# Performance work log

Measured on AMD Instinct MI355X. Metric: run time of the kernel, lower is better.

Reference implementation:

```python
import jax, jax.numpy as jnp
import numpy as np

DIM = 768
HEADS = 12
DIM_HEAD = 64
INNER = HEADS * DIM_HEAD  # 768
SCALE = DIM_HEAD ** -0.5


def setup_inputs() -> dict:
    key = jax.random.key(0)
    k1, k2, k3, k4 = jax.random.split(key, 4)
    b, n = 8, 1024
    x = jax.random.normal(k1, (b, n, DIM), dtype=jnp.float32)
    # fused QKV projection, no bias: y = x @ w_qkv  -> [b, n, 3*inner]
    w_qkv = jax.random.normal(k2, (DIM, 3 * INNER), dtype=jnp.float32) * (DIM ** -0.5)
    # output projection with bias
    w_out = jax.random.normal(k3, (INNER, DIM), dtype=jnp.float32) * (INNER ** -0.5)
    b_out = jax.random.normal(k4, (DIM,), dtype=jnp.float32) * 0.02
    return {"x": x, "w_qkv": w_qkv, "w_out": w_out, "b_out": b_out}


def reference(x, w_qkv, w_out, b_out):
    b, n, _ = x.shape
    qkv = jnp.einsum('bnd,de->bne', x, w_qkv)  # [b, n, 3*inner]
    q, k, v = jnp.split(qkv, 3, axis=-1)
    # 'b n (h d) -> b h n d'
    def split_heads(t):
        return t.reshape(b, n, HEADS, DIM_HEAD).transpose(0, 2, 1, 3)
    q, k, v = split_heads(q), split_heads(k), split_heads(v)
    dots = jnp.einsum('bhid,bhjd->bhij', q, k) * SCALE  # [b, h, n, n]
    attn = jax.nn.softmax(dots, axis=-1)
    out = jnp.einsum('bhij,bhjd->bhid', attn, v)  # [b, h, n, d]
    out = out.transpose(0, 2, 1, 3).reshape(b, n, INNER)  # 'b h n d -> b n (h d)'
    return jnp.einsum('bne,ed->bnd', out, w_out) + b_out
```

## Files before the change

kernel.cpp:

```cpp
#include <hip/hip_runtime.h>

typedef unsigned short u16;
typedef __bf16 bf16x8 __attribute__((ext_vector_type(8)));
typedef float f32x4 __attribute__((ext_vector_type(4)));

__device__ inline u16 f2bf(float f) {
    union { float f; unsigned int u; } a; a.f = f;
    unsigned int u = a.u + 0x7fffu + ((a.u >> 16) & 1u);
    return (u16)(u >> 16);
}

__device__ __forceinline__ void cp16(const void* g, void* l) {
    __builtin_amdgcn_global_load_lds(
        (const __attribute__((address_space(1))) unsigned int*)g,
        (__attribute__((address_space(3))) unsigned int*)l, 16, 0, 0);
}

__global__ __launch_bounds__(256) void prep(
    const float* __restrict__ x, const float* __restrict__ wq,
    const float* __restrict__ wo, u16* __restrict__ xbf,
    u16* __restrict__ wtq, u16* __restrict__ wto)
{
    int bid = blockIdx.x;
    if (bid < 3072) {
        size_t base = ((size_t)bid * 256 + threadIdx.x) * 8;
        float4 f0 = *(const float4*)&x[base];
        float4 f1 = *(const float4*)&x[base + 4];
        union { u16 s[8]; uint4 v; } t;
        t.s[0]=f2bf(f0.x); t.s[1]=f2bf(f0.y); t.s[2]=f2bf(f0.z); t.s[3]=f2bf(f0.w);
        t.s[4]=f2bf(f1.x); t.s[5]=f2bf(f1.y); t.s[6]=f2bf(f1.z); t.s[7]=f2bf(f1.w);
        *(uint4*)&xbf[base] = t.v;
        return;
    }
    __shared__ u16 tile[32][33];
    const float* in; u16* outp; int N, bx, by;
    if (bid < 3072 + 1728) { int t = bid - 3072; in = wq; outp = wtq; N = 2304; bx = t % 72; by = t / 72; }
    else                   { int t = bid - 4800; in = wo; outp = wto; N = 768;  bx = t % 24; by = t / 24; }
    int n0 = bx * 32, k0 = by * 32;
    int tx = threadIdx.x & 31, ty = threadIdx.x >> 5;
    #pragma unroll
    for (int r = ty; r < 32; r += 8)
        tile[r][tx] = f2bf(in[(size_t)(k0 + r) * N + n0 + tx]);
    __syncthreads();
    #pragma unroll
    for (int r = ty; r < 32; r += 8)
        outp[(size_t)(n0 + r) * 768 + k0 + tx] = tile[tx][r];
}

__global__ __launch_bounds__(256) void gemm_qkv(
    const u16* __restrict__ A, const u16* __restrict__ Bt,
    u16* __restrict__ q_out, u16* __restrict__ k_out, u16* __restrict__ v_out)
{
    const int K = 768;
    __shared__ __align__(16) u16 As[2][128 * 64];
    __shared__ __align__(16) u16 Bs[2][128 * 64];

    int tid = threadIdx.x;
    int lane = tid & 63, wave = tid >> 6;
    int quad = lane >> 4, l16 = lane & 15;
    int wm = wave >> 1, wn = wave & 1;
    int id = blockIdx.x;
    int xcd = id & 7, j = id >> 3;
    int m0 = (((j & 7) << 3) + xcd) * 128;
    int n0 = (j >> 3) * 128;

    f32x4 acc[4][4];
    #pragma unroll
    for (int i = 0; i < 4; i++)
        #pragma unroll
        for (int jj = 0; jj < 4; jj++) acc[i][jj] = (f32x4){0.f, 0.f, 0.f, 0.f};

    int r0 = tid >> 3, cg = tid & 7;
    int g = cg ^ (r0 & 7);
    const u16* GA[4]; const u16* GB[4];
    #pragma unroll
    for (int it = 0; it < 4; it++) {
        GA[it] = A  + (size_t)(m0 + it * 32 + r0) * K + g * 8;
        GB[it] = Bt + (size_t)(n0 + it * 32 + r0) * K + g * 8;
    }

    #define STAGE_QKV(kt, b)                                          \
        _Pragma("unroll")                                             \
        for (int it = 0; it < 4; it++) {                              \
            cp16(GA[it] + (kt), &As[b][(it * 256 + tid) * 8]);        \
            cp16(GB[it] + (kt), &Bs[b][(it * 256 + tid) * 8]);        \
        }

    STAGE_QKV(0, 0)
    for (int i = 0; i < 12; i++) {
        int b = i & 1;
        if (i + 1 < 12) {
            STAGE_QKV((i + 1) * 64, b ^ 1)
            asm volatile("s_waitcnt vmcnt(8)" ::: "memory");
        } else {
            asm volatile("s_waitcnt vmcnt(0)" ::: "memory");
        }
        __builtin_amdgcn_s_barrier();
        bf16x8 af[2][4], bfr[2][4];
        #pragma unroll
        for (int ko = 0; ko < 2; ko++)
            #pragma unroll
            for (int x = 0; x < 4; x++) {
                int Ra = wm * 64 + x * 16 + l16;
                af[ko][x]  = *(const bf16x8*)&As[b][Ra * 64 + (((ko * 4 + quad) ^ (Ra & 7)) * 8)];
                int Rb = wn * 64 + x * 16 + l16;
                bfr[ko][x] = *(const bf16x8*)&Bs[b][Rb * 64 + (((ko * 4 + quad) ^ (Rb & 7)) * 8)];
            }
        #pragma unroll
        for (int ko = 0; ko < 2; ko++)
            #pragma unroll
            for (int x = 0; x < 4; x++)
                #pragma unroll
                for (int y = 0; y < 4; y++)
                    acc[x][y] = __builtin_amdgcn_mfma_f32_16x16x32_bf16(af[ko][x], bfr[ko][y], acc[x][y], 0, 0, 0);
        __builtin_amdgcn_s_barrier();
    }
    #undef STAGE_QKV

    int M0 = m0 + wm * 64, N0 = n0 + wn * 64;
    int part = N0 >= 1536 ? 2 : (N0 >= 768 ? 1 : 0);
    int h = (N0 - part * 768) >> 6;
    int b2 = M0 >> 10, npos0 = M0 & 1023;
    u16* ep = (wave < 2 ? As[0] : Bs[0]) + (wave & 1) * 4096;

    if (part != 2) {
        float scale = (part == 0) ? 0.18033688011112042f : 1.0f;
        u16* gbase = (part == 0 ? q_out : k_out) + (((size_t)(b2 * 12 + h) * 1024 + npos0) << 6);
        #pragma unroll
        for (int i = 0; i < 4; i++)
            #pragma unroll
            for (int jj = 0; jj < 4; jj++) {
                int dd = jj * 16 + l16;
                #pragma unroll
                for (int r = 0; r < 4; r++) {
                    int np = i * 16 + quad * 4 + r;
                    ep[np * 64 + (((dd >> 3) ^ (np & 7)) * 8) + (dd & 7)] =
                        f2bf(acc[i][jj][r] * scale);
                }
            }
        #pragma unroll
        for (int t = 0; t < 8; t++) {
            int idx = t * 512 + lane * 8;
            int np = idx >> 6;
            int slot = ((lane & 7) ^ (np & 7));
            uint4 v = *(const uint4*)&ep[np * 64 + slot * 8];
            *(uint4*)&gbase[idx] = v;
        }
    } else {
        #pragma unroll
        for (int i = 0; i < 4; i++)
            #pragma unroll
            for (int jj = 0; jj < 4; jj++) {
                int dd = jj * 16 + l16;
                int npg = i * 2 + (quad >> 1);
                int sub = (quad & 1) * 4;
                union { u16 s[4]; uint2 v; } pk;
                #pragma unroll
                for (int r = 0; r < 4; r++) pk.s[r] = f2bf(acc[i][jj][r]);
                *(uint2*)&ep[dd * 64 + ((npg ^ (dd & 7)) * 8) + sub] = pk.v;
            }
        #pragma unroll
        for (int t = 0; t < 8; t++) {
            int dd = t * 8 + (lane >> 3);
            int npg = lane & 7;
            uint4 v = *(const uint4*)&ep[dd * 64 + ((npg ^ (dd & 7)) * 8)];
            *(uint4*)&v_out[((size_t)((b2 * 12 + h) * 64 + dd)) * 1024 + npos0 + npg * 8] = v;
        }
    }
}

__global__ __launch_bounds__(256) void attn128(
    u16* __restrict__ QO, const u16* __restrict__ Kg, const u16* __restrict__ Vtg)
{
    __shared__ __align__(16) u16 Ks[2][64 * 64];
    __shared__ __align__(16) u16 Vs[2][64 * 64];

    int tid = threadIdx.x;
    int lane = tid & 63, wave = tid >> 6;
    int quad = lane >> 4, l16 = lane & 15;
    int id = blockIdx.x;
    int xcd = id & 7, j = id >> 3;
    int bh = xcd * 12 + (j >> 3);
    int q0 = (j & 7) * 128;
    const size_t head_base = (size_t)bh * 65536;

    size_t qoff[2];
    bf16x8 qf[2][2];
    #pragma unroll
    for (int qs = 0; qs < 2; qs++) {
        qoff[qs] = head_base + (size_t)(q0 + wave * 32 + qs * 16 + l16) * 64;
        qf[qs][0] = *(const bf16x8*)&QO[qoff[qs] + quad * 8];
        qf[qs][1] = *(const bf16x8*)&QO[qoff[qs] + 32 + quad * 8];
    }

    f32x4 Oacc[4][2];
    #pragma unroll
    for (int dt = 0; dt < 4; dt++)
        #pragma unroll
        for (int qs = 0; qs < 2; qs++) Oacc[dt][qs] = (f32x4){0.f, 0.f, 0.f, 0.f};
    f32x4 lacc[2];
    lacc[0] = (f32x4){0.f, 0.f, 0.f, 0.f};
    lacc[1] = (f32x4){0.f, 0.f, 0.f, 0.f};

    union { unsigned int w[4]; bf16x8 v; } ones;
    ones.w[0] = ones.w[1] = ones.w[2] = ones.w[3] = 0x3f803f80u;

    int srow = tid >> 3, sg = tid & 7;
    int gsK = sg ^ (srow & 7);
    const u16* GK[2];
    GK[0] = Kg + head_base + (size_t)(srow) * 64 + gsK * 8;
    GK[1] = Kg + head_base + (size_t)(32 + srow) * 64 + gsK * 8;
    const u16* GV[2];
    GV[0] = Vtg + head_base + (size_t)(srow) * 1024 + sg * 8;
    GV[1] = Vtg + head_base + (size_t)(32 + srow) * 1024 + sg * 8;
    int vwA[2], vwB[2];
    #pragma unroll
    for (int it = 0; it < 2; it++) {
        int r = it * 32 + srow;
        vwA[it] = r * 64 + (((2 * sg)     ^ (r & 15)) * 4);
        vwB[it] = r * 64 + (((2 * sg + 1) ^ (r & 15)) * 4);
    }

    uint4 v0a = *(const uint4*)GV[0];
    uint4 v0b = *(const uint4*)GV[1];
    cp16(GK[0], &Ks[0][(0 * 256 + tid) * 8]);
    cp16(GK[1], &Ks[0][(1 * 256 + tid) * 8]);
    { uint2 t;
      t.x = v0a.x; t.y = v0a.y; *(uint2*)&Vs[0][vwA[0]] = t;
      t.x = v0a.z; t.y = v0a.w; *(uint2*)&Vs[0][vwB[0]] = t;
      t.x = v0b.x; t.y = v0b.y; *(uint2*)&Vs[0][vwA[1]] = t;
      t.x = v0b.z; t.y = v0b.w; *(uint2*)&Vs[0][vwB[1]] = t; }
    asm volatile("s_waitcnt lgkmcnt(0)" ::: "memory");

    for (int i = 0; i < 16; i++) {
        int b = i & 1;
        uint4 vna, vnb;
        if (i + 1 < 16) {
            vna = *(const uint4*)(GV[0] + (i + 1) * 64);
            vnb = *(const uint4*)(GV[1] + (i + 1) * 64);
            cp16(GK[0] + (size_t)(i + 1) * 4096, &Ks[b ^ 1][(0 * 256 + tid) * 8]);
            cp16(GK[1] + (size_t)(i + 1) * 4096, &Ks[b ^ 1][(1 * 256 + tid) * 8]);
            asm volatile("s_waitcnt vmcnt(4)" ::: "memory");
        } else {
            asm volatile("s_waitcnt vmcnt(0)" ::: "memory");
        }
        __builtin_amdgcn_s_barrier();

        bf16x8 kf[4][2];
        #pragma unroll
        for (int nt = 0; nt < 4; nt++) {
            int R = nt * 16 + l16;
            kf[nt][0] = *(const bf16x8*)&Ks[b][R * 64 + ((quad       ^ (R & 7)) * 8)];
            kf[nt][1] = *(const bf16x8*)&Ks[b][R * 64 + (((quad + 4) ^ (R & 7)) * 8)];
        }
        f32x4 s4[4][2];
        #pragma unroll
        for (int nt = 0; nt < 4; nt++)
            #pragma unroll
            for (int qs = 0; qs < 2; qs++) {
                f32x4 s = (f32x4){0.f, 0.f, 0.f, 0.f};
                s = __builtin_amdgcn_mfma_f32_16x16x32_bf16(kf[nt][0], qf[qs][0], s, 0, 0, 0);
                s = __builtin_amdgcn_mfma_f32_16x16x32_bf16(kf[nt][1], qf[qs][1], s, 0, 0, 0);
                s4[nt][qs] = s;
            }

        float p[4][2][4];
        #pragma unroll
        for (int nt = 0; nt < 4; nt++)
            #pragma unroll
            for (int qs = 0; qs < 2; qs++)
                #pragma unroll
                for (int r = 0; r < 4; r++)
                    p[nt][qs][r] = __builtin_amdgcn_exp2f(s4[nt][qs][r]);

        if (i + 1 < 16) {
            asm volatile("s_waitcnt vmcnt(2)" ::: "memory");
            uint2 t;
            t.x = vna.x; t.y = vna.y; *(uint2*)&Vs[b ^ 1][vwA[0]] = t;
            t.x = vna.z; t.y = vna.w; *(uint2*)&Vs[b ^ 1][vwB[0]] = t;
            t.x = vnb.x; t.y = vnb.y; *(uint2*)&Vs[b ^ 1][vwA[1]] = t;
            t.x = vnb.z; t.y = vnb.w; *(uint2*)&Vs[b ^ 1][vwB[1]] = t;
        }

        __builtin_amdgcn_s_setprio(1);
        #pragma unroll
        for (int h = 0; h < 2; h++) {
            union { unsigned int w[4]; bf16x8 v; } pk[2];
            #pragma unroll
            for (int qs = 0; qs < 2; qs++) {
                asm("v_cvt_pk_bf16_f32 %0, %1, %2" : "=v"(pk[qs].w[0]) : "v"(p[2*h][qs][0]),     "v"(p[2*h][qs][1]));
                asm("v_cvt_pk_bf16_f32 %0, %1, %2" : "=v"(pk[qs].w[1]) : "v"(p[2*h][qs][2]),     "v"(p[2*h][qs][3]));
                asm("v_cvt_pk_bf16_f32 %0, %1, %2" : "=v"(pk[qs].w[2]) : "v"(p[2*h+1][qs][0]),   "v"(p[2*h+1][qs][1]));
                asm("v_cvt_pk_bf16_f32 %0, %1, %2" : "=v"(pk[qs].w[3]) : "v"(p[2*h+1][qs][2]),   "v"(p[2*h+1][qs][3]));
                lacc[qs] = __builtin_amdgcn_mfma_f32_16x16x32_bf16(ones.v, pk[qs].v, lacc[qs], 0, 0, 0);
            }
            int pbase = ((8 * h + quad) ^ l16) * 4;
            #pragma unroll
            for (int dt = 0; dt < 4; dt++) {
                int drow = dt * 16 + l16;
                union { u16 s[8]; bf16x8 v; } vk;
                *(uint2*)&vk.s[0] = *(const uint2*)&Vs[b][drow * 64 + pbase];
                *(uint2*)&vk.s[4] = *(const uint2*)&Vs[b][drow * 64 + (pbase ^ 16)];
                #pragma unroll
                for (int qs = 0; qs < 2; qs++)
                    Oacc[dt][qs] = __builtin_amdgcn_mfma_f32_16x16x32_bf16(vk.v, pk[qs].v, Oacc[dt][qs], 0, 0, 0);
            }
        }
        __builtin_amdgcn_s_setprio(0);

        asm volatile("s_waitcnt lgkmcnt(0)" ::: "memory");
        __builtin_amdgcn_s_barrier();
    }

    #pragma unroll
    for (int qs = 0; qs < 2; qs++) {
        float rl = __builtin_amdgcn_rcpf(lacc[qs][0]);
        #pragma unroll
        for (int dt = 0; dt < 4; dt++) {
            union { u16 s[4]; uint2 v; } ok;
            #pragma unroll
            for (int r = 0; r < 4; r++) ok.s[r] = f2bf(Oacc[dt][qs][r] * rl);
            *(uint2*)&QO[qoff[qs] + dt * 16 + quad * 4] = ok.v;
        }
    }
}

__global__ __launch_bounds__(256) void gemm_out(
    const u16* __restrict__ Qg, const u16* __restrict__ Bt,
    const float* __restrict__ bias, float* __restrict__ out)
{
    const int K = 768;
    __shared__ __align__(16) u16 As[2][128 * 64];
    __shared__ __align__(16) u16 Bs[2][128 * 64];

    int tid = threadIdx.x;
    int lane = tid & 63, wave = tid >> 6;
    int quad = lane >> 4, l16 = lane & 15;
    int wm = wave >> 1, wn = wave & 1;
    int id = blockIdx.x;
    int xcd = id & 7, j = id >> 3;
    int m0 = (((j & 7) << 3) + xcd) * 128;
    int n0 = (j >> 3) * 128;

    f32x4 acc[4][4];
    #pragma unroll
    for (int i = 0; i < 4; i++)
        #pragma unroll
        for (int jj = 0; jj < 4; jj++) acc[i][jj] = (f32x4){0.f, 0.f, 0.f, 0.f};

    int r0 = tid >> 3, cg = tid & 7;
    int g = cg ^ (r0 & 7);
    const u16* GA[4]; const u16* GB[4];
    #pragma unroll
    for (int it = 0; it < 4; it++) {
        int m = m0 + it * 32 + r0, b = m >> 10, npos = m & 1023;
        GA[it] = Qg + (((size_t)(b * 12) * 1024 + npos) << 6) + g * 8;
        GB[it] = Bt + (size_t)(n0 + it * 32 + r0) * K + g * 8;
    }

    #define STAGE_OUT(i2, b)                                              \
        _Pragma("unroll")                                                 \
        for (int it = 0; it < 4; it++) {                                  \
            cp16(GA[it] + (size_t)(i2) * 65536, &As[b][(it * 256 + tid) * 8]); \
            cp16(GB[it] + (i2) * 64,            &Bs[b][(it * 256 + tid) * 8]); \
        }

    STAGE_OUT(0, 0)
    for (int i = 0; i < 12; i++) {
        int b = i & 1;
        if (i + 1 < 12) {
            STAGE_OUT(i + 1, b ^ 1)
            asm volatile("s_waitcnt vmcnt(8)" ::: "memory");
        } else {
            asm volatile("s_waitcnt vmcnt(0)" ::: "memory");
        }
        __builtin_amdgcn_s_barrier();
        bf16x8 af[2][4], bfr[2][4];
        #pragma unroll
        for (int ko = 0; ko < 2; ko++)
            #pragma unroll
            for (int x = 0; x < 4; x++) {
                int Ra = wm * 64 + x * 16 + l16;
                af[ko][x]  = *(const bf16x8*)&As[b][Ra * 64 + (((ko * 4 + quad) ^ (Ra & 7)) * 8)];
                int Rb = wn * 64 + x * 16 + l16;
                bfr[ko][x] = *(const bf16x8*)&Bs[b][Rb * 64 + (((ko * 4 + quad) ^ (Rb & 7)) * 8)];
            }
        #pragma unroll
        for (int ko = 0; ko < 2; ko++)
            #pragma unroll
            for (int x = 0; x < 4; x++)
                #pragma unroll
                for (int y = 0; y < 4; y++)
                    acc[x][y] = __builtin_amdgcn_mfma_f32_16x16x32_bf16(af[ko][x], bfr[ko][y], acc[x][y], 0, 0, 0);
        __builtin_amdgcn_s_barrier();
    }
    #undef STAGE_OUT

    #pragma unroll
    for (int i = 0; i < 4; i++) {
        int mbase = m0 + wm * 64 + i * 16 + quad * 4;
        #pragma unroll
        for (int jj = 0; jj < 4; jj++) {
            int n = n0 + wn * 64 + jj * 16 + l16;
            float bv = bias[n];
            #pragma unroll
            for (int r = 0; r < 4; r++)
                out[(size_t)(mbase + r) * 768 + n] = acc[i][jj][r] + bv;
        }
    }
}

extern "C" void kernel_launch(void* const* d_in, const int* in_sizes, int n_in,
                              void* d_out, int out_size, void* d_ws, size_t ws_size,
                              hipStream_t stream) {
    const float* x     = (const float*)d_in[0];
    const float* w_qkv = (const float*)d_in[1];
    const float* w_out = (const float*)d_in[2];
    const float* b_out = (const float*)d_in[3];
    float* out = (float*)d_out;

    char* ws = (char*)d_ws;
    u16* wtq  = (u16*)(ws);
    u16* wto  = (u16*)(ws + 3538944);
    u16* Qbuf = (u16*)(ws + 4718592);
    u16* xbf  = (u16*)(ws + 17301504);
    u16* Kbuf = (u16*)d_out;
    u16* Vbuf = (u16*)d_out + 6291456;

    prep<<<dim3(5376), 256, 0, stream>>>(x, w_qkv, w_out, xbf, wtq, wto);
    gemm_qkv<<<dim3(1152), 256, 0, stream>>>(xbf, wtq, Qbuf, Kbuf, Vbuf);
    attn128<<<dim3(768), 256, 0, stream>>>(Qbuf, Kbuf, Vbuf);
    gemm_out<<<dim3(384), 256, 0, stream>>>(Qbuf, wto, b_out, out);
}
```

Before: 192.4 us.

## Prefetch V tiles two iterations ahead with register ping-pong in attention loop

Restructures the attention main loop into a manually unrolled pair of stages. V global loads are now issued two tiles ahead into alternating register sets, while K still goes one tile ahead via direct-to-LDS copies. The V LDS write for the next tile moves to the start of compute, so the in-loop vmcnt wait before the P·V stage goes away and global latency gets more cover. The cost is extra live registers for the second V buffer and more code size from the unrolling.

```diff
diff --git a/kernel.cpp b/kernel.cpp
--- a/kernel.cpp
+++ b/kernel.cpp
@@ -221,96 +221,115 @@
         vwB[it] = r * 64 + (((2 * sg + 1) ^ (r & 15)) * 4);
     }
 
-    uint4 v0a = *(const uint4*)GV[0];
-    uint4 v0b = *(const uint4*)GV[1];
+    uint4 vA0, vA1, vB0, vB1;
+
+    {
+        uint4 t0 = *(const uint4*)GV[0];
+        uint4 t1 = *(const uint4*)GV[1];
+        uint2 t;
+        t.x = t0.x; t.y = t0.y; *(uint2*)&Vs[0][vwA[0]] = t;
+        t.x = t0.z; t.y = t0.w; *(uint2*)&Vs[0][vwB[0]] = t;
+        t.x = t1.x; t.y = t1.y; *(uint2*)&Vs[0][vwA[1]] = t;
+        t.x = t1.z; t.y = t1.w; *(uint2*)&Vs[0][vwB[1]] = t;
+    }
+    vA0 = *(const uint4*)(GV[0] + 64);
+    vA1 = *(const uint4*)(GV[1] + 64);
     cp16(GK[0], &Ks[0][(0 * 256 + tid) * 8]);
     cp16(GK[1], &Ks[0][(1 * 256 + tid) * 8]);
-    { uint2 t;
-      t.x = v0a.x; t.y = v0a.y; *(uint2*)&Vs[0][vwA[0]] = t;
-      t.x = v0a.z; t.y = v0a.w; *(uint2*)&Vs[0][vwB[0]] = t;
-      t.x = v0b.x; t.y = v0b.y; *(uint2*)&Vs[0][vwA[1]] = t;
-      t.x = v0b.z; t.y = v0b.w; *(uint2*)&Vs[0][vwB[1]] = t; }
     asm volatile("s_waitcnt lgkmcnt(0)" ::: "memory");
 
-    for (int i = 0; i < 16; i++) {
-        int b = i & 1;
-        uint4 vna, vnb;
-        if (i + 1 < 16) {
-            vna = *(const uint4*)(GV[0] + (i + 1) * 64);
-            vnb = *(const uint4*)(GV[1] + (i + 1) * 64);
-            cp16(GK[0] + (size_t)(i + 1) * 4096, &Ks[b ^ 1][(0 * 256 + tid) * 8]);
-            cp16(GK[1] + (size_t)(i + 1) * 4096, &Ks[b ^ 1][(1 * 256 + tid) * 8]);
-            asm volatile("s_waitcnt vmcnt(4)" ::: "memory");
-        } else {
-            asm volatile("s_waitcnt vmcnt(0)" ::: "memory");
-        }
-        __builtin_amdgcn_s_barrier();
-
-        bf16x8 kf[4][2];
-        #pragma unroll
-        for (int nt = 0; nt < 4; nt++) {
-            int R = nt * 16 + l16;
-            kf[nt][0] = *(const bf16x8*)&Ks[b][R * 64 + ((quad       ^ (R & 7)) * 8)];
-            kf[nt][1] = *(const bf16x8*)&Ks[b][R * 64 + (((quad + 4) ^ (R & 7)) * 8)];
-        }
-        f32x4 s4[4][2];
-        #pragma unroll
-        for (int nt = 0; nt < 4; nt++)
-            #pragma unroll
-            for (int qs = 0; qs < 2; qs++) {
-                f32x4 s = (f32x4){0.f, 0.f, 0.f, 0.f};
-                s = __builtin_amdgcn_mfma_f32_16x16x32_bf16(kf[nt][0], qf[qs][0], s, 0, 0, 0);
-                s = __builtin_amdgcn_mfma_f32_16x16x32_bf16(kf[nt][1], qf[qs][1], s, 0, 0, 0);
-                s4[nt][qs] = s;
-            }
-
-        float p[4][2][4];
-        #pragma unroll
-        for (int nt = 0; nt < 4; nt++)
-            #pragma unroll
-            for (int qs = 0; qs < 2; qs++)
-                #pragma unroll
-                for (int r = 0; r < 4; r++)
-                    p[nt][qs][r] = __builtin_amdgcn_exp2f(s4[nt][qs][r]);
-
-        if (i + 1 < 16) {
-            asm volatile("s_waitcnt vmcnt(2)" ::: "memory");
-            uint2 t;
-            t.x = vna.x; t.y = vna.y; *(uint2*)&Vs[b ^ 1][vwA[0]] = t;
-            t.x = vna.z; t.y = vna.w; *(uint2*)&Vs[b ^ 1][vwB[0]] = t;
-            t.x = vnb.x; t.y = vnb.y; *(uint2*)&Vs[b ^ 1][vwA[1]] = t;
-            t.x = vnb.z; t.y = vnb.w; *(uint2*)&Vs[b ^ 1][vwB[1]] = t;
-        }
-
-        __builtin_amdgcn_s_setprio(1);
-        #pragma unroll
-        for (int h = 0; h < 2; h++) {
-            union { unsigned int w[4]; bf16x8 v; } pk[2];
-            #pragma unroll
-            for (int qs = 0; qs < 2; qs++) {
-                asm("v_cvt_pk_bf16_f32 %0, %1, %2" : "=v"(pk[qs].w[0]) : "v"(p[2*h][qs][0]),     "v"(p[2*h][qs][1]));
-                asm("v_cvt_pk_bf16_f32 %0, %1, %2" : "=v"(pk[qs].w[1]) : "v"(p[2*h][qs][2]),     "v"(p[2*h][qs][3]));
-                asm("v_cvt_pk_bf16_f32 %0, %1, %2" : "=v"(pk[qs].w[2]) : "v"(p[2*h+1][qs][0]),   "v"(p[2*h+1][qs][1]));
-                asm("v_cvt_pk_bf16_f32 %0, %1, %2" : "=v"(pk[qs].w[3]) : "v"(p[2*h+1][qs][2]),   "v"(p[2*h+1][qs][3]));
-                lacc[qs] = __builtin_amdgcn_mfma_f32_16x16x32_bf16(ones.v, pk[qs].v, lacc[qs], 0, 0, 0);
-            }
-            int pbase = ((8 * h + quad) ^ l16) * 4;
-            #pragma unroll
-            for (int dt = 0; dt < 4; dt++) {
-                int drow = dt * 16 + l16;
-                union { u16 s[8]; bf16x8 v; } vk;
-                *(uint2*)&vk.s[0] = *(const uint2*)&Vs[b][drow * 64 + pbase];
-                *(uint2*)&vk.s[4] = *(const uint2*)&Vs[b][drow * 64 + (pbase ^ 16)];
-                #pragma unroll
-                for (int qs = 0; qs < 2; qs++)
-                    Oacc[dt][qs] = __builtin_amdgcn_mfma_f32_16x16x32_bf16(vk.v, pk[qs].v, Oacc[dt][qs], 0, 0, 0);
-            }
-        }
-        __builtin_amdgcn_s_setprio(0);
-
-        asm volatile("s_waitcnt lgkmcnt(0)" ::: "memory");
-        __builtin_amdgcn_s_barrier();
-    }
+    #define ATT_PF(I, PFV, PFK, VN0, VN1)                                        \
+        if (PFV) {                                                               \
+            VN0 = *(const uint4*)(GV[0] + ((I) + 2) * 64);                       \
+            VN1 = *(const uint4*)(GV[1] + ((I) + 2) * 64);                       \
+        }                                                                        \
+        if (PFK) {                                                               \
+            cp16(GK[0] + (size_t)((I) + 1) * 4096, &Ks[((I) + 1) & 1][(0 * 256 + tid) * 8]); \
+            cp16(GK[1] + (size_t)((I) + 1) * 4096, &Ks[((I) + 1) & 1][(1 * 256 + tid) * 8]); \
+        }
+
+    #define ATT_COMP(I, WRV, VC0, VC1)                                           \
+    {                                                                            \
+        int b = (I) & 1;                                                         \
+        __builtin_amdgcn_s_barrier();                                            \
+        bf16x8 kf[4][2];                                                         \
+        _Pragma("unroll")                                                        \
+        for (int nt = 0; nt < 4; nt++) {                                         \
+            int R = nt * 16 + l16;                                               \
+            kf[nt][0] = *(const bf16x8*)&Ks[b][R * 64 + ((quad       ^ (R & 7)) * 8)]; \
+            kf[nt][1] = *(const bf16x8*)&Ks[b][R * 64 + (((quad + 4) ^ (R & 7)) * 8)]; \
+        }                                                                        \
+        if (WRV) {                                                               \
+            uint2 t;                                                             \
+            t.x = VC0.x; t.y = VC0.y; *(uint2*)&Vs[b ^ 1][vwA[0]] = t;           \
+            t.x = VC0.z; t.y = VC0.w; *(uint2*)&Vs[b ^ 1][vwB[0]] = t;           \
+            t.x = VC1.x; t.y = VC1.y; *(uint2*)&Vs[b ^ 1][vwA[1]] = t;           \
+            t.x = VC1.z; t.y = VC1.w; *(uint2*)&Vs[b ^ 1][vwB[1]] = t;           \
+        }                                                                        \
+        f32x4 s4[4][2];                                                          \
+        _Pragma("unroll")                                                        \
+        for (int nt = 0; nt < 4; nt++)                                           \
+            _Pragma("unroll")                                                    \
+            for (int qs = 0; qs < 2; qs++) {                                     \
+                f32x4 s = (f32x4){0.f, 0.f, 0.f, 0.f};                           \
+                s = __builtin_amdgcn_mfma_f32_16x16x32_bf16(kf[nt][0], qf[qs][0], s, 0, 0, 0); \
+                s = __builtin_amdgcn_mfma_f32_16x16x32_bf16(kf[nt][1], qf[qs][1], s, 0, 0, 0); \
+                s4[nt][qs] = s;                                                  \
+            }                                                                    \
+        float p[4][2][4];                                                        \
+        _Pragma("unroll")                                                        \
+        for (int nt = 0; nt < 4; nt++)                                           \
+            _Pragma("unroll")                                                    \
+            for (int qs = 0; qs < 2; qs++)                                       \
+                _Pragma("unroll")                                                \
+                for (int r = 0; r < 4; r++)                                      \
+                    p[nt][qs][r] = __builtin_amdgcn_exp2f(s4[nt][qs][r]);        \
+        __builtin_amdgcn_s_setprio(1);                                           \
+        _Pragma("unroll")                                                        \
+        for (int h = 0; h < 2; h++) {                                            \
+            union { unsigned int w[4]; bf16x8 v; } pk[2];                        \
+            _Pragma("unroll")                                                    \
+            for (int qs = 0; qs < 2; qs++) {                                     \
+                asm("v_cvt_pk_bf16_f32 %0, %1, %2" : "=v"(pk[qs].w[0]) : "v"(p[2*h][qs][0]),   "v"(p[2*h][qs][1])); \
+                asm("v_cvt_pk_bf16_f32 %0, %1, %2" : "=v"(pk[qs].w[1]) : "v"(p[2*h][qs][2]),   "v"(p[2*h][qs][3])); \
+                asm("v_cvt_pk_bf16_f32 %0, %1, %2" : "=v"(pk[qs].w[2]) : "v"(p[2*h+1][qs][0]), "v"(p[2*h+1][qs][1])); \
+                asm("v_cvt_pk_bf16_f32 %0, %1, %2" : "=v"(pk[qs].w[3]) : "v"(p[2*h+1][qs][2]), "v"(p[2*h+1][qs][3])); \
+                lacc[qs] = __builtin_amdgcn_mfma_f32_16x16x32_bf16(ones.v, pk[qs].v, lacc[qs], 0, 0, 0); \
+            }                                                                    \
+            int pbase = ((8 * h + quad) ^ l16) * 4;                              \
+            _Pragma("unroll")                                                    \
+            for (int dt = 0; dt < 4; dt++) {                                     \
+                int drow = dt * 16 + l16;                                        \
+                union { u16 s[8]; bf16x8 v; } vk;                                \
+                *(uint2*)&vk.s[0] = *(const uint2*)&Vs[b][drow * 64 + pbase];    \
+                *(uint2*)&vk.s[4] = *(const uint2*)&Vs[b][drow * 64 + (pbase ^ 16)]; \
+                _Pragma("unroll")                                                \
+                for (int qs = 0; qs < 2; qs++)                                   \
+                    Oacc[dt][qs] = __builtin_amdgcn_mfma_f32_16x16x32_bf16(vk.v, pk[qs].v, Oacc[dt][qs], 0, 0, 0); \
+            }                                                                    \
+        }                                                                        \
+        __builtin_amdgcn_s_setprio(0);                                           \
+        asm volatile("s_waitcnt lgkmcnt(0)" ::: "memory");                       \
+        __builtin_amdgcn_s_barrier();                                            \
+    }
+
+    for (int ii = 0; ii < 7; ii++) {
+        int i0 = 2 * ii, i1 = i0 + 1;
+        ATT_PF(i0, 1, 1, vB0, vB1)
+        asm volatile("s_waitcnt vmcnt(4)" ::: "memory");
+        ATT_COMP(i0, 1, vA0, vA1)
+        ATT_PF(i1, 1, 1, vA0, vA1)
+        asm volatile("s_waitcnt vmcnt(4)" ::: "memory");
+        ATT_COMP(i1, 1, vB0, vB1)
+    }
+    ATT_PF(14, 0, 1, vB0, vB1)
+    asm volatile("s_waitcnt vmcnt(2)" ::: "memory");
+    ATT_COMP(14, 1, vA0, vA1)
+    asm volatile("s_waitcnt vmcnt(0)" ::: "memory");
+    ATT_COMP(15, 0, vB0, vB1)
+
+    #undef ATT_PF
+    #undef ATT_COMP
 
     #pragma unroll
     for (int qs = 0; qs < 2; qs++) {
```

Result: faster. 187.7 us (-2.5%).
